# Kernel tuning notes

Hardware: AMD Instinct MI355X
Metric: run time of the kernel (lower is better)

## Reference

```python
import jax, jax.numpy as jnp
import numpy as np

B, T, S = 64, 32, 64          # batch, tgt_len, src_len
V, E, H, C = 32000, 512, 1024, 2048  # vocab, emb, hidden, context (2*d_model)


def setup_inputs() -> dict:
    key = jax.random.key(0)
    ks = jax.random.split(key, 16)
    g = lambda i, shape, s=0.05: jax.random.normal(ks[i], shape, jnp.float32) * s
    return dict(
        y=jax.random.randint(ks[0], (B, T), 0, V),
        context=g(1, (B, S, C), 1.0),
        context_mask=jnp.zeros((B, S), jnp.int32),  # 1 = padding
        hidden=g(2, (B, H), 1.0),
        emb=g(3, (V, E)),
        W_ih1=g(4, (3 * H, E)), W_hh1=g(5, (3 * H, H)),
        b_ih1=jnp.zeros((3 * H,), jnp.float32), b_hh1=jnp.zeros((3 * H,), jnp.float32),
        Wq=g(6, (H, H)), bq=jnp.zeros((H,), jnp.float32),
        Wk=g(7, (C, H)), v_attn=g(8, (H,)),
        W_ih2=g(9, (3 * H, C)), W_hh2=g(10, (3 * H, H)),
        b_ih2=jnp.zeros((3 * H,), jnp.float32), b_hh2=jnp.zeros((3 * H,), jnp.float32),
        Wi=g(11, (E, E)), bi=jnp.zeros((E,), jnp.float32),
        Wh=g(12, (E, H)), bh=jnp.zeros((E,), jnp.float32),
        Wc=g(13, (E, C)), bc=jnp.zeros((E,), jnp.float32),
    )


def gru_cell(x, h, W_ih, W_hh, b_ih, b_hh):
    gi = x @ W_ih.T + b_ih
    gh = h @ W_hh.T + b_hh
    i_r, i_z, i_n = jnp.split(gi, 3, axis=-1)
    h_r, h_z, h_n = jnp.split(gh, 3, axis=-1)
    r = jax.nn.sigmoid(i_r + h_r)
    z = jax.nn.sigmoid(i_z + h_z)
    n = jnp.tanh(i_n + r * h_n)
    return (1.0 - z) * n + z * h


def reference(y, context, context_mask, hidden, emb,
              W_ih1, W_hh1, b_ih1, b_hh1,
              Wq, bq, Wk, v_attn,
              W_ih2, W_hh2, b_ih2, b_hh2,
              Wi, bi, Wh, bh, Wc, bc):
    x = emb[y]                                        # [B,T,E]
    cache = jnp.einsum('bsc,ch->bsh', context, Wk)    # attention key cache
    pad = context_mask.astype(bool)
    neg = jnp.finfo(x.dtype).min

    def step(h, x_t):
        h1 = gru_cell(x_t, h, W_ih1, W_hh1, b_ih1, b_hh1)        # [B,H]
        q = h1 @ Wq + bq                                          # [B,H]
        scores = jnp.einsum('bsh,h->bs', jnp.tanh(q[:, None, :] + cache), v_attn)
        probs = jax.nn.softmax(jnp.where(pad, neg, scores), axis=-1)
        attn = jnp.einsum('bs,bsc->bc', probs, context)           # [B,C]
        h2 = gru_cell(attn, h1, W_ih2, W_hh2, b_ih2, b_hh2)
        return h2, (h2, attn)

    h_final, (out, attn) = jax.lax.scan(step, hidden, jnp.swapaxes(x, 0, 1))
    out = jnp.swapaxes(out, 0, 1)                     # [B,T,H]
    attn = jnp.swapaxes(attn, 0, 1)                   # [B,T,C]
    logits = jnp.tanh(x @ Wi.T + bi + out @ Wh.T + bh + attn @ Wc.T + bc)
    return logits, h_final
```

## Files before the change

kernel.cpp:

```cpp
#include <hip/hip_runtime.h>
#include <math.h>

#define B_ 64
#define T_ 32
#define S_ 64
#define E_ 512
#define H_ 1024
#define C_ 2048
#define G_ 3072
#define NBLK 256
#define FLSTR 16

typedef __bf16 bf16_t;
typedef bf16_t bf16x8 __attribute__((ext_vector_type(8)));
typedef float f32x4 __attribute__((ext_vector_type(4)));
typedef unsigned long long u64;

__device__ __forceinline__ float sigm_(float x) { return 1.f / (1.f + __expf(-x)); }
__device__ __forceinline__ float tanh_(float x) { return 1.f - 2.f / (__expf(2.f * x) + 1.f); }

__device__ __forceinline__ unsigned short bits_(bf16_t x)
{
    union { bf16_t b; unsigned short u; } c; c.b = x; return c.u;
}
__device__ __forceinline__ void astore_pair(bf16_t* p, bf16_t lo, bf16_t hi)
{
    unsigned u = (unsigned)bits_(lo) | ((unsigned)bits_(hi) << 16);
    __hip_atomic_store((unsigned*)p, u, __ATOMIC_RELAXED, __HIP_MEMORY_SCOPE_AGENT);
}
__device__ __forceinline__ void astore_f32(float* p, float v)
{
    union { float f; unsigned u; } c; c.f = v;
    __hip_atomic_store((unsigned*)p, c.u, __ATOMIC_RELAXED, __HIP_MEMORY_SCOPE_AGENT);
}

__device__ __forceinline__ void split8(const float* __restrict__ p, bf16x8& h, bf16x8& l)
{
    float4 a = *(const float4*)p;
    float4 b = *(const float4*)(p + 4);
    float v[8] = {a.x, a.y, a.z, a.w, b.x, b.y, b.z, b.w};
    #pragma unroll
    for (int q = 0; q < 8; ++q) {
        h[q] = (bf16_t)v[q];
        l[q] = (bf16_t)(v[q] - (float)h[q]);
    }
}

__global__ __launch_bounds__(256)
void embed_kernel(const int* __restrict__ y, const float* __restrict__ emb,
                  float* __restrict__ x)
{
    int i = blockIdx.x * 256 + threadIdx.x;
    int row = i / (E_ / 4);
    int e4  = i % (E_ / 4);
    const float4* src = (const float4*)(emb + (size_t)y[row] * E_);
    ((float4*)(x + (size_t)row * E_))[e4] = src[e4];
}

__global__ void transpose_kernel(const float* __restrict__ in, float* __restrict__ out,
                                 int R, int Ccols)
{
    __shared__ float t[32][33];
    int r0 = blockIdx.y * 32, c0 = blockIdx.x * 32;
    t[threadIdx.y][threadIdx.x] = in[(size_t)(r0 + threadIdx.y) * Ccols + c0 + threadIdx.x];
    __syncthreads();
    out[(size_t)(c0 + threadIdx.y) * R + r0 + threadIdx.x] = t[threadIdx.x][threadIdx.y];
}

__global__ __launch_bounds__(256)
void cvt_ctx(const float* __restrict__ in, bf16_t* __restrict__ out)
{
    int i = blockIdx.x * 256 + threadIdx.x;
    const float4* s4 = (const float4*)in + 2 * i;
    float4 a = s4[0], b = s4[1];
    bf16x8 o;
    o[0] = (bf16_t)a.x; o[1] = (bf16_t)a.y; o[2] = (bf16_t)a.z; o[3] = (bf16_t)a.w;
    o[4] = (bf16_t)b.x; o[5] = (bf16_t)b.y; o[6] = (bf16_t)b.z; o[7] = (bf16_t)b.w;
    ((bf16x8*)out)[i] = o;
}

#define LSTR 80

template<int ACCUM, int PERM>
__global__ __launch_bounds__(256)
void sgemm(const float* __restrict__ A, const float* __restrict__ Wt,
           float* __restrict__ out, int N, int K)
{
    __shared__ char AH[128 * LSTR];
    __shared__ char AL[128 * LSTR];
    __shared__ char WH[128 * LSTR];
    __shared__ char WL[128 * LSTR];
    const int tid = threadIdx.x;
    const int lane = tid & 63, wave = tid >> 6;
    const int m0 = blockIdx.y * 128, n0 = blockIdx.x * 128;
    const int wm = (wave & 1) * 64, wn = (wave >> 1) * 64;
    const int l15 = lane & 15, l4 = lane >> 4;

    f32x4 acc[4][4] = {};

    for (int k0 = 0; k0 < K; k0 += 32) {
        #pragma unroll
        for (int p = 0; p < 2; ++p) {
            int e = tid + p * 256;
            int row = e >> 2, ch = e & 3;
            int off = row * LSTR + ch * 16;
            bf16x8 h, l;
            split8(A + (size_t)(m0 + row) * K + k0 + ch * 8, h, l);
            *(bf16x8*)(AH + off) = h; *(bf16x8*)(AL + off) = l;
            split8(Wt + (size_t)(n0 + row) * K + k0 + ch * 8, h, l);
            *(bf16x8*)(WH + off) = h; *(bf16x8*)(WL + off) = l;
        }
        __syncthreads();
        bf16x8 ah[4], al[4], wh[4], wl[4];
        #pragma unroll
        for (int i = 0; i < 4; ++i) {
            int off = (wm + i * 16 + l15) * LSTR + l4 * 16;
            ah[i] = *(const bf16x8*)(AH + off);
            al[i] = *(const bf16x8*)(AL + off);
        }
        #pragma unroll
        for (int j = 0; j < 4; ++j) {
            int off = (wn + j * 16 + l15) * LSTR + l4 * 16;
            wh[j] = *(const bf16x8*)(WH + off);
            wl[j] = *(const bf16x8*)(WL + off);
        }
        #pragma unroll
        for (int i = 0; i < 4; ++i)
            #pragma unroll
            for (int j = 0; j < 4; ++j) {
                acc[i][j] = __builtin_amdgcn_mfma_f32_16x16x32_bf16(ah[i], wh[j], acc[i][j], 0, 0, 0);
                acc[i][j] = __builtin_amdgcn_mfma_f32_16x16x32_bf16(ah[i], wl[j], acc[i][j], 0, 0, 0);
                acc[i][j] = __builtin_amdgcn_mfma_f32_16x16x32_bf16(al[i], wh[j], acc[i][j], 0, 0, 0);
            }
        __syncthreads();
    }

    #pragma unroll
    for (int i = 0; i < 4; ++i)
        #pragma unroll
        for (int j = 0; j < 4; ++j)
            #pragma unroll
            for (int r = 0; r < 4; ++r) {
                int m = m0 + wm + i * 16 + l4 * 4 + r;
                int n = n0 + wn + j * 16 + l15;
                if (PERM) {
                    int b = m >> 5, t = m & 31;
                    int gate = n >> 10, jj = n & 1023;
                    size_t dst = (((size_t)(jj >> 2) * 32 + t) * 64 + b) * 12
                                 + gate * 4 + (jj & 3);
                    out[dst] = acc[i][j][r];
                } else if (ACCUM) {
                    out[(size_t)m * N + n] += acc[i][j][r];
                } else {
                    out[(size_t)m * N + n] = acc[i][j][r];
                }
            }
}

#define W1H_OFF 0
#define W1L_OFF 24576
#define W3H_OFF 49152
#define W2H_OFF 98304
#define W2L_OFF 131072
#define SMEM_BYTES 163840

__device__ __forceinline__ void gbar(unsigned* flags, unsigned* done,
                                     unsigned epoch, int blk, int tid)
{
    asm volatile("s_waitcnt vmcnt(0)" ::: "memory");
    __syncthreads();
    if (blk == 0) {
        if (tid > 0 && tid < NBLK) {
            while (__hip_atomic_load(&flags[tid * FLSTR], __ATOMIC_RELAXED,
                                     __HIP_MEMORY_SCOPE_AGENT) < epoch)
                __builtin_amdgcn_s_sleep(4);
        }
        __syncthreads();
        if (tid < 8)
            __hip_atomic_store(&done[tid * FLSTR], epoch, __ATOMIC_RELAXED,
                               __HIP_MEMORY_SCOPE_AGENT);
        __syncthreads();
    } else {
        if (tid == 0) {
            __hip_atomic_store(&flags[blk * FLSTR], epoch, __ATOMIC_RELAXED,
                               __HIP_MEMORY_SCOPE_AGENT);
            while (__hip_atomic_load(&done[(blk & 7) * FLSTR], __ATOMIC_RELAXED,
                                     __HIP_MEMORY_SCOPE_AGENT) < epoch)
                __builtin_amdgcn_s_sleep(4);
        }
        __syncthreads();
    }
}

__global__ __launch_bounds__(1024, 4)
void scan_kernel(
    const float* __restrict__ Whh1, const float* __restrict__ Whh2,
    const float* __restrict__ WqT,  const float* __restrict__ Wih2,
    const float* __restrict__ xg2,
    const float* __restrict__ b_ih1, const float* __restrict__ b_hh1,
    const float* __restrict__ b_ih2, const float* __restrict__ b_hh2,
    const float* __restrict__ bq,    const float* __restrict__ v_attn,
    const int*   __restrict__ cmask,
    const float* __restrict__ hidden,
    const float* __restrict__ cacheK, const bf16_t* __restrict__ ctxb,
    float* __restrict__ qgv, float* __restrict__ hf,
    bf16_t* __restrict__ h1H, bf16_t* __restrict__ h1L,
    float* __restrict__ attnseq, float* __restrict__ outseq,
    float* __restrict__ hfinal,
    float* __restrict__ scgv,
    unsigned* __restrict__ flags, unsigned* __restrict__ done)
{
    extern __shared__ char sm[];
    const int tid = threadIdx.x, blk = blockIdx.x;
    const int lane = tid & 63, wave = tid >> 6;
    const int l15 = lane & 15, l4 = lane >> 4;
    const int blk4 = blk * 4;
    const int ab  = blk & 63;
    const int aq  = blk >> 6;

    if (tid == 0) __builtin_amdgcn_fence(__ATOMIC_ACQUIRE, "agent");
    __syncthreads();

    for (int e = tid; e < 12 * 128; e += 1024) {
        int r = e >> 7, c = e & 127;
        bf16x8 h, l;
        split8(Whh1 + (size_t)((r >> 2) * 1024 + blk4 + (r & 3)) * 1024 + c * 8, h, l);
        int off = r * 2048 + ((c * 16) ^ ((r & 7) << 4));
        *(bf16x8*)(sm + W1H_OFF + off) = h;
        *(bf16x8*)(sm + W1L_OFF + off) = l;
    }
    for (int e = tid; e < 16 * 128; e += 1024) {
        int r = e >> 7, c = e & 127;
        const float* src = (r < 12)
            ? Whh2 + (size_t)((r >> 2) * 1024 + blk4 + (r & 3)) * 1024 + c * 8
            : WqT + (size_t)(blk4 + r - 12) * 1024 + c * 8;
        bf16x8 h, l;
        split8(src, h, l);
        int off = r * 2048 + ((c * 16) ^ ((r & 7) << 4));
        *(bf16x8*)(sm + W2H_OFF + off) = h;
        *(bf16x8*)(sm + W2L_OFF + off) = l;
    }
    for (int e = tid; e < 12 * 256; e += 1024) {
        int r = e >> 8, c = e & 255;
        bf16x8 h, l;
        split8(Wih2 + (size_t)((r >> 2) * 1024 + blk4 + (r & 3)) * 2048 + c * 8, h, l);
        *(bf16x8*)(sm + W3H_OFF + r * 4096 + ((c * 16) ^ ((r & 7) << 4))) = h;
    }

    const int j = blk4 + l15;
    if (wave < 4 && l15 < 4) {
        #pragma unroll
        for (int r2 = 0; r2 < 4; ++r2) {
            int b = wave * 16 + l4 * 4 + r2;
            hf[b * 1024 + j] = hidden[b * 1024 + j];
        }
    }

    float vreg[16], bqreg[16];
    #pragma unroll
    for (int i = 0; i < 16; ++i) {
        vreg[i]  = v_attn[lane + 64 * i];
        bqreg[i] = bq[lane + 64 * i];
    }
    float ckreg[16];
    {
        const float* ck = cacheK + ((size_t)ab * 64 + aq * 16 + wave) * 1024;
        #pragma unroll
        for (int i = 0; i < 16; ++i) ckreg[i] = ck[lane + 64 * i];
    }
    const int cmy = aq * 512 + (tid >> 1);
    const int sbase = (tid & 1) * 32;
    unsigned cr[16];
    {
        const bf16_t* cb = ctxb + ((size_t)ab * 64 + sbase) * 2048 + cmy;
        #pragma unroll
        for (int q = 0; q < 16; ++q) {
            unsigned lo = bits_(cb[(size_t)(2 * q) * 2048]);
            unsigned hi = bits_(cb[(size_t)(2 * q + 1) * 2048]);
            cr[q] = lo | (hi << 16);
        }
    }

    float bi1r = 0, bi1z = 0, bi1n = 0, bh1r = 0, bh1z = 0, bh1n = 0;
    float bi2r = 0, bi2z = 0, bi2n = 0, bh2r = 0, bh2z = 0, bh2n = 0;
    if (wave < 4 && l15 < 4) {
        bi1r = b_ih1[j]; bi1z = b_ih1[1024 + j]; bi1n = b_ih1[2048 + j];
        bh1r = b_hh1[j]; bh1z = b_hh1[1024 + j]; bh1n = b_hh1[2048 + j];
        bi2r = b_ih2[j]; bi2z = b_ih2[1024 + j]; bi2n = b_ih2[2048 + j];
        bh2r = b_hh2[j]; bh2z = b_hh2[1024 + j]; bh2n = b_hh2[2048 + j];
    }

    unsigned epoch = 0;
    gbar(flags, done, ++epoch, blk, tid);

    float h1r_[4] = {0.f, 0.f, 0.f, 0.f};
    f32x4 acc1 = {0.f, 0.f, 0.f, 0.f};

    for (int t = 0; t < T_; ++t) {
        if (wave < 4) {
            f32x4 acc0 = {0.f, 0.f, 0.f, 0.f};
            const int brow = wave * 16 + l15;
            const float* asrc = (t == 0) ? hidden + (size_t)brow * 1024
                                         : outseq + ((size_t)brow * T_ + t - 1) * 1024;
            #pragma unroll 8
            for (int kk = 0; kk < 32; ++kk) {
                bf16x8 avh, avl;
                split8(asrc + kk * 32 + l4 * 8, avh, avl);
                int boff = (kk * 64 + l4 * 16) ^ ((l15 & 7) << 4);
                bf16x8 bvh = *(const bf16x8*)(sm + W1H_OFF + l15 * 2048 + boff);
                bf16x8 bvl = *(const bf16x8*)(sm + W1L_OFF + l15 * 2048 + boff);
                acc0 = __builtin_amdgcn_mfma_f32_16x16x32_bf16(avh, bvh, acc0, 0, 0, 0);
                acc0 = __builtin_amdgcn_mfma_f32_16x16x32_bf16(avl, bvh, acc0, 0, 0, 0);
                acc0 = __builtin_amdgcn_mfma_f32_16x16x32_bf16(avh, bvl, acc0, 0, 0, 0);
            }
            const float* xg = xg2 + (((size_t)blk * 32 + t) * 64) * 12;
            #pragma unroll
            for (int r2 = 0; r2 < 4; ++r2) {
                float gr = acc0[r2];
                float gz = __shfl(acc0[r2], (lane & 48) | (l15 + 4), 64);
                float gn = __shfl(acc0[r2], (lane & 48) | (l15 + 8), 64);
                float h1v = 0.f;
                int b = wave * 16 + l4 * 4 + r2;
                if (l15 < 4) {
                    float rr = sigm_(xg[b * 12 + l15]     + bi1r + gr + bh1r);
                    float zz = sigm_(xg[b * 12 + 4 + l15] + bi1z + gz + bh1z);
                    float nn = tanh_(xg[b * 12 + 8 + l15] + bi1n + rr * (gn + bh1n));
                    h1v = (1.f - zz) * nn + zz * hf[b * 1024 + j];
                    h1r_[r2] = h1v;
                }
                float h1o = __shfl(h1v, lane + 1, 64);
                if (l15 < 4 && (l15 & 1) == 0) {
                    bf16_t hS = (bf16_t)h1v, hO = (bf16_t)h1o;
                    size_t vo = ((size_t)t * 64 + b) * 1024 + j;
                    astore_pair(h1H + vo, hS, hO);
                    astore_pair(h1L + vo,
                                (bf16_t)(h1v - (float)hS), (bf16_t)(h1o - (float)hO));
                }
            }
        }
        gbar(flags, done, ++epoch, blk, tid);

        if (wave < 4) {
            acc1 = (f32x4){0.f, 0.f, 0.f, 0.f};
            const int brow = wave * 16 + l15;
            const bf16_t* ah = h1H + ((size_t)t * 64 + brow) * 1024;
            const bf16_t* al = h1L + ((size_t)t * 64 + brow) * 1024;
            #pragma unroll 8
            for (int kk = 0; kk < 32; ++kk) {
                bf16x8 avh = *(const bf16x8*)(ah + kk * 32 + l4 * 8);
                bf16x8 avl = *(const bf16x8*)(al + kk * 32 + l4 * 8);
                int boff = (kk * 64 + l4 * 16) ^ ((l15 & 7) << 4);
                bf16x8 bvh = *(const bf16x8*)(sm + W2H_OFF + l15 * 2048 + boff);
                bf16x8 bvl = *(const bf16x8*)(sm + W2L_OFF + l15 * 2048 + boff);
                acc1 = __builtin_amdgcn_mfma_f32_16x16x32_bf16(avh, bvh, acc1, 0, 0, 0);
                acc1 = __builtin_amdgcn_mfma_f32_16x16x32_bf16(avl, bvh, acc1, 0, 0, 0);
                acc1 = __builtin_amdgcn_mfma_f32_16x16x32_bf16(avh, bvl, acc1, 0, 0, 0);
            }
            if (l15 >= 12) {
                int jq = blk4 + l15 - 12;
                #pragma unroll
                for (int r2 = 0; r2 < 4; ++r2)
                    astore_f32(&qgv[((size_t)t * 64 + (wave * 16 + l4 * 4 + r2)) * 1024 + jq],
                               acc1[r2]);
            }
        }
        gbar(flags, done, ++epoch, blk, tid);

        {
            const float* qrow = qgv + ((size_t)t * 64 + ab) * 1024;
            float sum = 0.f;
            #pragma unroll
            for (int i = 0; i < 16; ++i)
                sum += tanh_(qrow[lane + 64 * i] + bqreg[i] + ckreg[i]) * vreg[i];
            #pragma unroll
            for (int off = 32; off; off >>= 1) sum += __shfl_down(sum, off, 64);
            if (lane == 0) astore_f32(&scgv[(size_t)t * 4096 + ab * 64 + aq * 16 + wave], sum);
        }
        gbar(flags, done, ++epoch, blk, tid);

        {
            const float* scrow = scgv + (size_t)t * 4096 + ab * 64;
            float v = (cmask[ab * 64 + lane] != 0) ? -3.4e38f : scrow[lane];
            float mx = v;
            #pragma unroll
            for (int off = 32; off; off >>= 1) mx = fmaxf(mx, __shfl_xor(mx, off, 64));
            float e = __expf(v - mx);
            float sden = e;
            #pragma unroll
            for (int off = 32; off; off >>= 1) sden += __shfl_xor(sden, off, 64);
            float prv = e / sden;

            float sum = 0.f;
            #pragma unroll
            for (int q = 0; q < 16; ++q) {
                float p0 = __shfl(prv, sbase + 2 * q, 64);
                float p1 = __shfl(prv, sbase + 2 * q + 1, 64);
                sum += p0 * __uint_as_float(cr[q] << 16);
                sum += p1 * __uint_as_float(cr[q] & 0xffff0000u);
            }
            sum += __shfl_xor(sum, 1, 64);
            if ((tid & 1) == 0)
                astore_f32(attnseq + ((size_t)ab * T_ + t) * 2048 + cmy, sum);
        }
        gbar(flags, done, ++epoch, blk, tid);

        if (wave < 4) {
            f32x4 acc3 = {0.f, 0.f, 0.f, 0.f};
            const int brow = wave * 16 + l15;
            const float* aptr = attnseq + ((size_t)brow * T_ + t) * 2048;
            #pragma unroll 8
            for (int kk = 0; kk < 64; ++kk) {
                bf16x8 avh, avl;
                split8(aptr + kk * 32 + l4 * 8, avh, avl);
                bf16x8 bvh = *(const bf16x8*)(sm + W3H_OFF + l15 * 4096 +
                                              ((kk * 64 + l4 * 16) ^ ((l15 & 7) << 4)));
                acc3 = __builtin_amdgcn_mfma_f32_16x16x32_bf16(avh, bvh, acc3, 0, 0, 0);
                acc3 = __builtin_amdgcn_mfma_f32_16x16x32_bf16(avl, bvh, acc3, 0, 0, 0);
            }
            #pragma unroll
            for (int r2 = 0; r2 < 4; ++r2) {
                float ir  = acc3[r2];
                float iz  = __shfl(acc3[r2], (lane & 48) | (l15 + 4), 64);
                float in2 = __shfl(acc3[r2], (lane & 48) | (l15 + 8), 64);
                float hr  = acc1[r2];
                float hz  = __shfl(acc1[r2], (lane & 48) | (l15 + 4), 64);
                float hn  = __shfl(acc1[r2], (lane & 48) | (l15 + 8), 64);
                int b = wave * 16 + l4 * 4 + r2;
                if (l15 < 4) {
                    float rr = sigm_(ir + bi2r + hr + bh2r);
                    float zz = sigm_(iz + bi2z + hz + bh2z);
                    float nn = tanh_(in2 + bi2n + rr * (hn + bh2n));
                    float h2 = (1.f - zz) * nn + zz * h1r_[r2];
                    hf[b * 1024 + j] = h2;
                    astore_f32(&outseq[((size_t)b * T_ + t) * 1024 + j], h2);
                    if (t == T_ - 1) hfinal[b * 1024 + j] = h2;
                }
            }
        }
        gbar(flags, done, ++epoch, blk, tid);
    }
}

__global__ __launch_bounds__(256)
void final_kernel(const float* __restrict__ Lacc,
                  const float* __restrict__ bi, const float* __restrict__ bh,
                  const float* __restrict__ bc, float* __restrict__ out)
{
    int i = blockIdx.x * 256 + threadIdx.x;
    int e = i & 511;
    out[i] = tanh_(Lacc[i] + bi[e] + bh[e] + bc[e]);
}

extern "C" void kernel_launch(void* const* d_in, const int* in_sizes, int n_in,
                              void* d_out, int out_size, void* d_ws, size_t ws_size,
                              hipStream_t stream)
{
    const int*   y       = (const int*)  d_in[0];
    const float* context = (const float*)d_in[1];
    const int*   cmask   = (const int*)  d_in[2];
    const float* hidden  = (const float*)d_in[3];
    const float* emb     = (const float*)d_in[4];
    const float* W_ih1   = (const float*)d_in[5];
    const float* W_hh1   = (const float*)d_in[6];
    const float* b_ih1   = (const float*)d_in[7];
    const float* b_hh1   = (const float*)d_in[8];
    const float* Wq      = (const float*)d_in[9];
    const float* bq      = (const float*)d_in[10];
    const float* Wk      = (const float*)d_in[11];
    const float* v_attn  = (const float*)d_in[12];
    const float* W_ih2   = (const float*)d_in[13];
    const float* W_hh2   = (const float*)d_in[14];
    const float* b_ih2   = (const float*)d_in[15];
    const float* b_hh2   = (const float*)d_in[16];
    const float* Wi      = (const float*)d_in[17];
    const float* bi      = (const float*)d_in[18];
    const float* Wh      = (const float*)d_in[19];
    const float* bh      = (const float*)d_in[20];
    const float* Wc      = (const float*)d_in[21];
    const float* bc      = (const float*)d_in[22];

    char* ws = (char*)d_ws;
    size_t o = 0;
    auto alloc = [&](size_t bytes) { char* p = ws + o; o += (bytes + 255) & ~(size_t)255; return p; };
    unsigned* flags = (unsigned*)alloc(NBLK * FLSTR * 4);
    unsigned* done  = (unsigned*)alloc(8 * FLSTR * 4);
    float*  x       = (float*) alloc((size_t)2048 * 512 * 4);
    float*  WkT     = (float*) alloc((size_t)1024 * 2048 * 4);
    float*  WqT     = (float*) alloc((size_t)1024 * 1024 * 4);
    bf16_t* ctxb    = (bf16_t*)alloc((size_t)4096 * 2048 * 2);
    float*  xg2     = (float*) alloc((size_t)2048 * 3072 * 4);
    float*  Lacc    = (float*) alloc((size_t)2048 * 512 * 4);
    float*  cacheK  = (float*) alloc((size_t)4096 * 1024 * 4);
    float*  qgv     = (float*) alloc((size_t)T_ * 64 * 1024 * 4);
    float*  hf      = (float*) alloc((size_t)64 * 1024 * 4);
    bf16_t* h1H     = (bf16_t*)alloc((size_t)T_ * 64 * 1024 * 2);
    bf16_t* h1L     = (bf16_t*)alloc((size_t)T_ * 64 * 1024 * 2);
    float*  attnseq = (float*) alloc((size_t)2048 * 2048 * 4);
    float*  outseq  = (float*) alloc((size_t)2048 * 1024 * 4);
    float*  scgv    = (float*) alloc((size_t)T_ * 64 * 64 * 4);

    hipMemsetAsync(flags, 0, (NBLK * FLSTR + 8 * FLSTR) * 4, stream);

    embed_kernel<<<(B_*T_*E_/4 + 255)/256, 256, 0, stream>>>(y, emb, x);
    transpose_kernel<<<dim3(1024/32, 2048/32), dim3(32,32), 0, stream>>>(Wk, WkT, 2048, 1024);
    transpose_kernel<<<dim3(1024/32, 1024/32), dim3(32,32), 0, stream>>>(Wq, WqT, 1024, 1024);
    cvt_ctx<<<(4096*2048/8)/256, 256, 0, stream>>>(context, ctxb);

    sgemm<0, 1><<<dim3(G_/128, 16), 256, 0, stream>>>(x, W_ih1, xg2, G_, E_);
    sgemm<0, 0><<<dim3(E_/128, 16), 256, 0, stream>>>(x, Wi, Lacc, E_, E_);
    sgemm<0, 0><<<dim3(H_/128, 32), 256, 0, stream>>>(context, WkT, cacheK, H_, C_);

    hipFuncSetAttribute((const void*)scan_kernel, hipFuncAttributeMaxDynamicSharedMemorySize, SMEM_BYTES);
    scan_kernel<<<NBLK, 1024, SMEM_BYTES, stream>>>(
        W_hh1, W_hh2, WqT, W_ih2, xg2,
        b_ih1, b_hh1, b_ih2, b_hh2, bq, v_attn, cmask, hidden, cacheK, ctxb,
        qgv, hf, h1H, h1L, attnseq, outseq,
        (float*)d_out + (size_t)B_ * T_ * E_, scgv, flags, done);

    sgemm<1, 0><<<dim3(E_/128, 16), 256, 0, stream>>>(outseq, Wh, Lacc, E_, H_);
    sgemm<1, 0><<<dim3(E_/128, 16), 256, 0, stream>>>(attnseq, Wc, Lacc, E_, C_);

    final_kernel<<<(B_*T_*E_)/256, 256, 0, stream>>>(Lacc, bi, bh, bc, (float*)d_out);
}
```

Measured before the change: 3.134 ms.

## Split-K across all 16 waves in scan GEMMs and fuse score phase

Each per-step MFMA GEMM (GRU1 hidden, GRU2 hidden/query, GRU2 input) now splits its K range across four wave groups. Partials are reduced through a per-block global scratch buffer behind a block-level sync, so all 16 waves do matmul work instead of only 4. The attention score computation now has each block compute all 64 source scores for its batch row locally, which removes one grid-wide barrier per timestep and the global score buffer. The query bias is folded into the stored q. This trades extra __syncthreads, scratch traffic and redundant cacheK reads for shorter serial critical paths.

```diff
diff --git a/kernel.cpp b/kernel.cpp
--- a/kernel.cpp
+++ b/kernel.cpp
@@ -207,7 +207,7 @@
     bf16_t* __restrict__ h1H, bf16_t* __restrict__ h1L,
     float* __restrict__ attnseq, float* __restrict__ outseq,
     float* __restrict__ hfinal,
-    float* __restrict__ scgv,
+    float* __restrict__ red,
     unsigned* __restrict__ flags, unsigned* __restrict__ done)
 {
     extern __shared__ char sm[];
@@ -217,6 +217,9 @@
     const int blk4 = blk * 4;
     const int ab  = blk & 63;
     const int aq  = blk >> 6;
+    const int kg  = wave >> 2;
+    const int bg  = wave & 3;
+    float* redp = red + (size_t)blk * 4096;
 
     if (tid == 0) __builtin_amdgcn_fence(__ATOMIC_ACQUIRE, "agent");
     __syncthreads();
@@ -256,18 +259,9 @@
         }
     }
 
-    float vreg[16], bqreg[16];
+    float vreg[16];
     #pragma unroll
-    for (int i = 0; i < 16; ++i) {
-        vreg[i]  = v_attn[lane + 64 * i];
-        bqreg[i] = bq[lane + 64 * i];
-    }
-    float ckreg[16];
-    {
-        const float* ck = cacheK + ((size_t)ab * 64 + aq * 16 + wave) * 1024;
-        #pragma unroll
-        for (int i = 0; i < 16; ++i) ckreg[i] = ck[lane + 64 * i];
-    }
+    for (int i = 0; i < 16; ++i) vreg[i] = v_attn[lane + 64 * i];
     const int cmy = aq * 512 + (tid >> 1);
     const int sbase = (tid & 1) * 32;
     unsigned cr[16];
@@ -283,12 +277,14 @@
 
     float bi1r = 0, bi1z = 0, bi1n = 0, bh1r = 0, bh1z = 0, bh1n = 0;
     float bi2r = 0, bi2z = 0, bi2n = 0, bh2r = 0, bh2z = 0, bh2n = 0;
+    float bqv = 0.f;
     if (wave < 4 && l15 < 4) {
         bi1r = b_ih1[j]; bi1z = b_ih1[1024 + j]; bi1n = b_ih1[2048 + j];
         bh1r = b_hh1[j]; bh1z = b_hh1[1024 + j]; bh1n = b_hh1[2048 + j];
         bi2r = b_ih2[j]; bi2z = b_ih2[1024 + j]; bi2n = b_ih2[2048 + j];
         bh2r = b_hh2[j]; bh2z = b_hh2[1024 + j]; bh2n = b_hh2[2048 + j];
     }
+    if (wave < 4 && l15 >= 12) bqv = bq[blk4 + l15 - 12];
 
     unsigned epoch = 0;
     gbar(flags, done, ++epoch, blk, tid);
@@ -297,90 +293,115 @@
     f32x4 acc1 = {0.f, 0.f, 0.f, 0.f};
 
     for (int t = 0; t < T_; ++t) {
-        if (wave < 4) {
-            f32x4 acc0 = {0.f, 0.f, 0.f, 0.f};
-            const int brow = wave * 16 + l15;
+        {
+            f32x4 a0 = {0.f, 0.f, 0.f, 0.f};
+            const int brow = bg * 16 + l15;
             const float* asrc = (t == 0) ? hidden + (size_t)brow * 1024
                                          : outseq + ((size_t)brow * T_ + t - 1) * 1024;
-            #pragma unroll 8
-            for (int kk = 0; kk < 32; ++kk) {
+            #pragma unroll
+            for (int kq = 0; kq < 8; ++kq) {
+                int kk = kg * 8 + kq;
                 bf16x8 avh, avl;
                 split8(asrc + kk * 32 + l4 * 8, avh, avl);
                 int boff = (kk * 64 + l4 * 16) ^ ((l15 & 7) << 4);
                 bf16x8 bvh = *(const bf16x8*)(sm + W1H_OFF + l15 * 2048 + boff);
                 bf16x8 bvl = *(const bf16x8*)(sm + W1L_OFF + l15 * 2048 + boff);
-                acc0 = __builtin_amdgcn_mfma_f32_16x16x32_bf16(avh, bvh, acc0, 0, 0, 0);
-                acc0 = __builtin_amdgcn_mfma_f32_16x16x32_bf16(avl, bvh, acc0, 0, 0, 0);
-                acc0 = __builtin_amdgcn_mfma_f32_16x16x32_bf16(avh, bvl, acc0, 0, 0, 0);
-            }
-            const float* xg = xg2 + (((size_t)blk * 32 + t) * 64) * 12;
-            #pragma unroll
-            for (int r2 = 0; r2 < 4; ++r2) {
-                float gr = acc0[r2];
-                float gz = __shfl(acc0[r2], (lane & 48) | (l15 + 4), 64);
-                float gn = __shfl(acc0[r2], (lane & 48) | (l15 + 8), 64);
-                float h1v = 0.f;
-                int b = wave * 16 + l4 * 4 + r2;
-                if (l15 < 4) {
-                    float rr = sigm_(xg[b * 12 + l15]     + bi1r + gr + bh1r);
-                    float zz = sigm_(xg[b * 12 + 4 + l15] + bi1z + gz + bh1z);
-                    float nn = tanh_(xg[b * 12 + 8 + l15] + bi1n + rr * (gn + bh1n));
-                    h1v = (1.f - zz) * nn + zz * hf[b * 1024 + j];
-                    h1r_[r2] = h1v;
-                }
-                float h1o = __shfl(h1v, lane + 1, 64);
-                if (l15 < 4 && (l15 & 1) == 0) {
-                    bf16_t hS = (bf16_t)h1v, hO = (bf16_t)h1o;
-                    size_t vo = ((size_t)t * 64 + b) * 1024 + j;
-                    astore_pair(h1H + vo, hS, hO);
-                    astore_pair(h1L + vo,
-                                (bf16_t)(h1v - (float)hS), (bf16_t)(h1o - (float)hO));
+                a0 = __builtin_amdgcn_mfma_f32_16x16x32_bf16(avh, bvh, a0, 0, 0, 0);
+                a0 = __builtin_amdgcn_mfma_f32_16x16x32_bf16(avl, bvh, a0, 0, 0, 0);
+                a0 = __builtin_amdgcn_mfma_f32_16x16x32_bf16(avh, bvl, a0, 0, 0, 0);
+            }
+            if (kg) *(f32x4*)(redp + (size_t)wave * 256 + lane * 4) = a0;
+            __syncthreads();
+            if (wave < 4) {
+                #pragma unroll
+                for (int g = 1; g < 4; ++g) {
+                    f32x4 p = *(const f32x4*)(redp + (size_t)(g * 4 + wave) * 256 + lane * 4);
+                    a0[0] += p[0]; a0[1] += p[1]; a0[2] += p[2]; a0[3] += p[3];
+                }
+                const float* xg = xg2 + (((size_t)blk * 32 + t) * 64) * 12;
+                #pragma unroll
+                for (int r2 = 0; r2 < 4; ++r2) {
+                    float gr = a0[r2];
+                    float gz = __shfl(a0[r2], (lane & 48) | (l15 + 4), 64);
+                    float gn = __shfl(a0[r2], (lane & 48) | (l15 + 8), 64);
+                    float h1v = 0.f;
+                    int b = wave * 16 + l4 * 4 + r2;
+                    if (l15 < 4) {
+                        float rr = sigm_(xg[b * 12 + l15]     + bi1r + gr + bh1r);
+                        float zz = sigm_(xg[b * 12 + 4 + l15] + bi1z + gz + bh1z);
+                        float nn = tanh_(xg[b * 12 + 8 + l15] + bi1n + rr * (gn + bh1n));
+                        h1v = (1.f - zz) * nn + zz * hf[b * 1024 + j];
+                        h1r_[r2] = h1v;
+                    }
+                    float h1o = __shfl(h1v, lane + 1, 64);
+                    if (l15 < 4 && (l15 & 1) == 0) {
+                        bf16_t hS = (bf16_t)h1v, hO = (bf16_t)h1o;
+                        size_t vo = ((size_t)t * 64 + b) * 1024 + j;
+                        astore_pair(h1H + vo, hS, hO);
+                        astore_pair(h1L + vo,
+                                    (bf16_t)(h1v - (float)hS), (bf16_t)(h1o - (float)hO));
+                    }
                 }
             }
         }
         gbar(flags, done, ++epoch, blk, tid);
 
-        if (wave < 4) {
-            acc1 = (f32x4){0.f, 0.f, 0.f, 0.f};
-            const int brow = wave * 16 + l15;
+        {
+            f32x4 a1 = {0.f, 0.f, 0.f, 0.f};
+            const int brow = bg * 16 + l15;
             const bf16_t* ah = h1H + ((size_t)t * 64 + brow) * 1024;
             const bf16_t* al = h1L + ((size_t)t * 64 + brow) * 1024;
-            #pragma unroll 8
-            for (int kk = 0; kk < 32; ++kk) {
+            #pragma unroll
+            for (int kq = 0; kq < 8; ++kq) {
+                int kk = kg * 8 + kq;
                 bf16x8 avh = *(const bf16x8*)(ah + kk * 32 + l4 * 8);
                 bf16x8 avl = *(const bf16x8*)(al + kk * 32 + l4 * 8);
                 int boff = (kk * 64 + l4 * 16) ^ ((l15 & 7) << 4);
                 bf16x8 bvh = *(const bf16x8*)(sm + W2H_OFF + l15 * 2048 + boff);
                 bf16x8 bvl = *(const bf16x8*)(sm + W2L_OFF + l15 * 2048 + boff);
-                acc1 = __builtin_amdgcn_mfma_f32_16x16x32_bf16(avh, bvh, acc1, 0, 0, 0);
-                acc1 = __builtin_amdgcn_mfma_f32_16x16x32_bf16(avl, bvh, acc1, 0, 0, 0);
-                acc1 = __builtin_amdgcn_mfma_f32_16x16x32_bf16(avh, bvl, acc1, 0, 0, 0);
-            }
-            if (l15 >= 12) {
-                int jq = blk4 + l15 - 12;
-                #pragma unroll
-                for (int r2 = 0; r2 < 4; ++r2)
-                    astore_f32(&qgv[((size_t)t * 64 + (wave * 16 + l4 * 4 + r2)) * 1024 + jq],
-                               acc1[r2]);
+                a1 = __builtin_amdgcn_mfma_f32_16x16x32_bf16(avh, bvh, a1, 0, 0, 0);
+                a1 = __builtin_amdgcn_mfma_f32_16x16x32_bf16(avl, bvh, a1, 0, 0, 0);
+                a1 = __builtin_amdgcn_mfma_f32_16x16x32_bf16(avh, bvl, a1, 0, 0, 0);
+            }
+            if (kg) *(f32x4*)(redp + (size_t)wave * 256 + lane * 4) = a1;
+            __syncthreads();
+            if (wave < 4) {
+                acc1 = a1;
+                #pragma unroll
+                for (int g = 1; g < 4; ++g) {
+                    f32x4 p = *(const f32x4*)(redp + (size_t)(g * 4 + wave) * 256 + lane * 4);
+                    acc1[0] += p[0]; acc1[1] += p[1]; acc1[2] += p[2]; acc1[3] += p[3];
+                }
+                if (l15 >= 12) {
+                    int jq = blk4 + l15 - 12;
+                    #pragma unroll
+                    for (int r2 = 0; r2 < 4; ++r2)
+                        astore_f32(&qgv[((size_t)t * 64 + (wave * 16 + l4 * 4 + r2)) * 1024 + jq],
+                                   acc1[r2] + bqv);
+                }
             }
         }
         gbar(flags, done, ++epoch, blk, tid);
 
         {
             const float* qrow = qgv + ((size_t)t * 64 + ab) * 1024;
-            float sum = 0.f;
-            #pragma unroll
-            for (int i = 0; i < 16; ++i)
-                sum += tanh_(qrow[lane + 64 * i] + bqreg[i] + ckreg[i]) * vreg[i];
-            #pragma unroll
-            for (int off = 32; off; off >>= 1) sum += __shfl_down(sum, off, 64);
-            if (lane == 0) astore_f32(&scgv[(size_t)t * 4096 + ab * 64 + aq * 16 + wave], sum);
-        }
-        gbar(flags, done, ++epoch, blk, tid);
-
-        {
-            const float* scrow = scgv + (size_t)t * 4096 + ab * 64;
-            float v = (cmask[ab * 64 + lane] != 0) ? -3.4e38f : scrow[lane];
+            float qreg[16];
+            #pragma unroll
+            for (int i = 0; i < 16; ++i) qreg[i] = qrow[lane + 64 * i];
+            #pragma unroll
+            for (int sl = 0; sl < 4; ++sl) {
+                int s = wave * 4 + sl;
+                const float* ck = cacheK + ((size_t)ab * 64 + s) * 1024;
+                float sum = 0.f;
+                #pragma unroll
+                for (int i = 0; i < 16; ++i)
+                    sum += tanh_(qreg[i] + ck[lane + 64 * i]) * vreg[i];
+                #pragma unroll
+                for (int off = 32; off; off >>= 1) sum += __shfl_down(sum, off, 64);
+                if (lane == 0) redp[s] = sum;
+            }
+            __syncthreads();
+            float v = (cmask[ab * 64 + lane] != 0) ? -3.4e38f : redp[lane];
             float mx = v;
             #pragma unroll
             for (int off = 32; off; off >>= 1) mx = fmaxf(mx, __shfl_xor(mx, off, 64));
@@ -404,36 +425,46 @@
         }
         gbar(flags, done, ++epoch, blk, tid);
 
-        if (wave < 4) {
-            f32x4 acc3 = {0.f, 0.f, 0.f, 0.f};
-            const int brow = wave * 16 + l15;
+        {
+            f32x4 a3 = {0.f, 0.f, 0.f, 0.f};
+            const int brow = bg * 16 + l15;
             const float* aptr = attnseq + ((size_t)brow * T_ + t) * 2048;
-            #pragma unroll 8
-            for (int kk = 0; kk < 64; ++kk) {
+            #pragma unroll
+            for (int kq = 0; kq < 16; ++kq) {
+                int kk = kg * 16 + kq;
                 bf16x8 avh, avl;
                 split8(aptr + kk * 32 + l4 * 8, avh, avl);
                 bf16x8 bvh = *(const bf16x8*)(sm + W3H_OFF + l15 * 4096 +
                                               ((kk * 64 + l4 * 16) ^ ((l15 & 7) << 4)));
-                acc3 = __builtin_amdgcn_mfma_f32_16x16x32_bf16(avh, bvh, acc3, 0, 0, 0);
-                acc3 = __builtin_amdgcn_mfma_f32_16x16x32_bf16(avl, bvh, acc3, 0, 0, 0);
-            }
-            #pragma unroll
-            for (int r2 = 0; r2 < 4; ++r2) {
-                float ir  = acc3[r2];
-                float iz  = __shfl(acc3[r2], (lane & 48) | (l15 + 4), 64);
-                float in2 = __shfl(acc3[r2], (lane & 48) | (l15 + 8), 64);
-                float hr  = acc1[r2];
-                float hz  = __shfl(acc1[r2], (lane & 48) | (l15 + 4), 64);
-                float hn  = __shfl(acc1[r2], (lane & 48) | (l15 + 8), 64);
-                int b = wave * 16 + l4 * 4 + r2;
-                if (l15 < 4) {
-                    float rr = sigm_(ir + bi2r + hr + bh2r);
-                    float zz = sigm_(iz + bi2z + hz + bh2z);
-                    float nn = tanh_(in2 + bi2n + rr * (hn + bh2n));
-                    float h2 = (1.f - zz) * nn + zz * h1r_[r2];
-                    hf[b * 1024 + j] = h2;
-                    astore_f32(&outseq[((size_t)b * T_ + t) * 1024 + j], h2);
-                    if (t == T_ - 1) hfinal[b * 1024 + j] = h2;
+                a3 = __builtin_amdgcn_mfma_f32_16x16x32_bf16(avh, bvh, a3, 0, 0, 0);
+                a3 = __builtin_amdgcn_mfma_f32_16x16x32_bf16(avl, bvh, a3, 0, 0, 0);
+            }
+            if (kg) *(f32x4*)(redp + (size_t)wave * 256 + lane * 4) = a3;
+            __syncthreads();
+            if (wave < 4) {
+                #pragma unroll
+                for (int g = 1; g < 4; ++g) {
+                    f32x4 p = *(const f32x4*)(redp + (size_t)(g * 4 + wave) * 256 + lane * 4);
+                    a3[0] += p[0]; a3[1] += p[1]; a3[2] += p[2]; a3[3] += p[3];
+                }
+                #pragma unroll
+                for (int r2 = 0; r2 < 4; ++r2) {
+                    float ir  = a3[r2];
+                    float iz  = __shfl(a3[r2], (lane & 48) | (l15 + 4), 64);
+                    float in2 = __shfl(a3[r2], (lane & 48) | (l15 + 8), 64);
+                    float hr  = acc1[r2];
+                    float hz  = __shfl(acc1[r2], (lane & 48) | (l15 + 4), 64);
+                    float hn  = __shfl(acc1[r2], (lane & 48) | (l15 + 8), 64);
+                    int b = wave * 16 + l4 * 4 + r2;
+                    if (l15 < 4) {
+                        float rr = sigm_(ir + bi2r + hr + bh2r);
+                        float zz = sigm_(iz + bi2z + hz + bh2z);
+                        float nn = tanh_(in2 + bi2n + rr * (hn + bh2n));
+                        float h2 = (1.f - zz) * nn + zz * h1r_[r2];
+                        hf[b * 1024 + j] = h2;
+                        astore_f32(&outseq[((size_t)b * T_ + t) * 1024 + j], h2);
+                        if (t == T_ - 1) hfinal[b * 1024 + j] = h2;
+                    }
                 }
             }
         }
@@ -497,7 +528,7 @@
     bf16_t* h1L     = (bf16_t*)alloc((size_t)T_ * 64 * 1024 * 2);
     float*  attnseq = (float*) alloc((size_t)2048 * 2048 * 4);
     float*  outseq  = (float*) alloc((size_t)2048 * 1024 * 4);
-    float*  scgv    = (float*) alloc((size_t)T_ * 64 * 64 * 4);
+    float*  red     = (float*) alloc((size_t)NBLK * 4096 * 4);
 
     hipMemsetAsync(flags, 0, (NBLK * FLSTR + 8 * FLSTR) * 4, stream);
 
@@ -515,7 +546,7 @@
         W_hh1, W_hh2, WqT, W_ih2, xg2,
         b_ih1, b_hh1, b_ih2, b_hh2, bq, v_attn, cmask, hidden, cacheK, ctxb,
         qgv, hf, h1H, h1L, attnseq, outseq,
-        (float*)d_out + (size_t)B_ * T_ * E_, scgv, flags, done);
+        (float*)d_out + (size_t)B_ * T_ * E_, red, flags, done);
 
     sgemm<1, 0><<<dim3(E_/128, 16), 256, 0, stream>>>(outseq, Wh, Lacc, E_, H_);
     sgemm<1, 0><<<dim3(E_/128, 16), 256, 0, stream>>>(attnseq, Wc, Lacc, E_, C_);
```

Result: slower. 3.577 ms (+14.1%).

## Compute all attention scores per batch in-block to remove a grid barrier

Applied to the files above, without the earlier changes.

Each block now computes all 64 source scores for its batch row instead of only 16, so the softmax no longer has to wait for other blocks. That removes one grid-wide barrier per timestep and the global score exchange buffer. The trade is four times the tanh work per block, 64 cache registers per thread instead of 16, and redundant score computation across the four blocks that share a batch. The bq bias is folded into the q store, and scores go through a per-block global scratch buffer synchronised with __syncthreads.

```diff
diff --git a/kernel.cpp b/kernel.cpp
--- a/kernel.cpp
+++ b/kernel.cpp
@@ -207,7 +207,7 @@
     bf16_t* __restrict__ h1H, bf16_t* __restrict__ h1L,
     float* __restrict__ attnseq, float* __restrict__ outseq,
     float* __restrict__ hfinal,
-    float* __restrict__ scgv,
+    float* __restrict__ red,
     unsigned* __restrict__ flags, unsigned* __restrict__ done)
 {
     extern __shared__ char sm[];
@@ -217,6 +217,7 @@
     const int blk4 = blk * 4;
     const int ab  = blk & 63;
     const int aq  = blk >> 6;
+    float* redp = red + (size_t)blk * 1024;
 
     if (tid == 0) __builtin_amdgcn_fence(__ATOMIC_ACQUIRE, "agent");
     __syncthreads();
@@ -256,17 +257,15 @@
         }
     }
 
-    float vreg[16], bqreg[16];
+    float vreg[16];
     #pragma unroll
-    for (int i = 0; i < 16; ++i) {
-        vreg[i]  = v_attn[lane + 64 * i];
-        bqreg[i] = bq[lane + 64 * i];
-    }
-    float ckreg[16];
-    {
-        const float* ck = cacheK + ((size_t)ab * 64 + aq * 16 + wave) * 1024;
-        #pragma unroll
-        for (int i = 0; i < 16; ++i) ckreg[i] = ck[lane + 64 * i];
+    for (int i = 0; i < 16; ++i) vreg[i] = v_attn[lane + 64 * i];
+    float ckreg[4][16];
+    #pragma unroll
+    for (int sl = 0; sl < 4; ++sl) {
+        const float* ck = cacheK + ((size_t)ab * 64 + wave * 4 + sl) * 1024;
+        #pragma unroll
+        for (int i = 0; i < 16; ++i) ckreg[sl][i] = ck[lane + 64 * i];
     }
     const int cmy = aq * 512 + (tid >> 1);
     const int sbase = (tid & 1) * 32;
@@ -283,12 +282,14 @@
 
     float bi1r = 0, bi1z = 0, bi1n = 0, bh1r = 0, bh1z = 0, bh1n = 0;
     float bi2r = 0, bi2z = 0, bi2n = 0, bh2r = 0, bh2z = 0, bh2n = 0;
+    float bqv = 0.f;
     if (wave < 4 && l15 < 4) {
         bi1r = b_ih1[j]; bi1z = b_ih1[1024 + j]; bi1n = b_ih1[2048 + j];
         bh1r = b_hh1[j]; bh1z = b_hh1[1024 + j]; bh1n = b_hh1[2048 + j];
         bi2r = b_ih2[j]; bi2z = b_ih2[1024 + j]; bi2n = b_ih2[2048 + j];
         bh2r = b_hh2[j]; bh2z = b_hh2[1024 + j]; bh2n = b_hh2[2048 + j];
     }
+    if (wave < 4 && l15 >= 12) bqv = bq[blk4 + l15 - 12];
 
     unsigned epoch = 0;
     gbar(flags, done, ++epoch, blk, tid);
@@ -361,26 +362,29 @@
                 #pragma unroll
                 for (int r2 = 0; r2 < 4; ++r2)
                     astore_f32(&qgv[((size_t)t * 64 + (wave * 16 + l4 * 4 + r2)) * 1024 + jq],
-                               acc1[r2]);
+                               acc1[r2] + bqv);
             }
         }
         gbar(flags, done, ++epoch, blk, tid);
 
         {
             const float* qrow = qgv + ((size_t)t * 64 + ab) * 1024;
-            float sum = 0.f;
-            #pragma unroll
-            for (int i = 0; i < 16; ++i)
-                sum += tanh_(qrow[lane + 64 * i] + bqreg[i] + ckreg[i]) * vreg[i];
-            #pragma unroll
-            for (int off = 32; off; off >>= 1) sum += __shfl_down(sum, off, 64);
-            if (lane == 0) astore_f32(&scgv[(size_t)t * 4096 + ab * 64 + aq * 16 + wave], sum);
-        }
-        gbar(flags, done, ++epoch, blk, tid);
-
-        {
-            const float* scrow = scgv + (size_t)t * 4096 + ab * 64;
-            float v = (cmask[ab * 64 + lane] != 0) ? -3.4e38f : scrow[lane];
+            float qreg[16];
+            #pragma unroll
+            for (int i = 0; i < 16; ++i) qreg[i] = qrow[lane + 64 * i];
+            #pragma unroll
+            for (int sl = 0; sl < 4; ++sl) {
+                float sum = 0.f;
+                #pragma unroll
+                for (int i = 0; i < 16; ++i)
+                    sum += tanh_(qreg[i] + ckreg[sl][i]) * vreg[i];
+                #pragma unroll
+                for (int off = 32; off; off >>= 1) sum += __shfl_down(sum, off, 64);
+                if (lane == 0) redp[wave * 4 + sl] = sum;
+            }
+            asm volatile("s_waitcnt vmcnt(0)" ::: "memory");
+            __syncthreads();
+            float v = (cmask[ab * 64 + lane] != 0) ? -3.4e38f : redp[lane];
             float mx = v;
             #pragma unroll
             for (int off = 32; off; off >>= 1) mx = fmaxf(mx, __shfl_xor(mx, off, 64));
@@ -497,7 +501,7 @@
     bf16_t* h1L     = (bf16_t*)alloc((size_t)T_ * 64 * 1024 * 2);
     float*  attnseq = (float*) alloc((size_t)2048 * 2048 * 4);
     float*  outseq  = (float*) alloc((size_t)2048 * 1024 * 4);
-    float*  scgv    = (float*) alloc((size_t)T_ * 64 * 64 * 4);
+    float*  red     = (float*) alloc((size_t)NBLK * 1024 * 4);
 
     hipMemsetAsync(flags, 0, (NBLK * FLSTR + 8 * FLSTR) * 4, stream);
 
@@ -515,7 +519,7 @@
         W_hh1, W_hh2, WqT, W_ih2, xg2,
         b_ih1, b_hh1, b_ih2, b_hh2, bq, v_attn, cmask, hidden, cacheK, ctxb,
         qgv, hf, h1H, h1L, attnseq, outseq,
-        (float*)d_out + (size_t)B_ * T_ * E_, scgv, flags, done);
+        (float*)d_out + (size_t)B_ * T_ * E_, red, flags, done);
 
     sgemm<1, 0><<<dim3(E_/128, 16), 256, 0, stream>>>(outseq, Wh, Lacc, E_, H_);
     sgemm<1, 0><<<dim3(E_/128, 16), 256, 0, stream>>>(attnseq, Wc, Lacc, E_, C_);
```

Measured after the change: 3.546 ms. 1.13x slower.

## Prefetch next-phase operands into cache using idle waves and fold bq into q

Applied to the files above, without the earlier changes.

The idle waves (4-15) now read the data the next phase will consume, such as previous outputs, h1 split buffers and attention vectors, and discard the sums. The goal is to warm the cache so the active waves see fewer misses after each grid barrier. The query bias is added once when q is written, instead of being held in per-thread registers for every score. The key cache rows are loaded from memory inside the step rather than kept in registers, which frees registers at the cost of extra loads. The prefetches add memory traffic that may compete with the active waves.

```diff
diff --git a/kernel.cpp b/kernel.cpp
--- a/kernel.cpp
+++ b/kernel.cpp
@@ -256,18 +256,9 @@
         }
     }
 
-    float vreg[16], bqreg[16];
+    float vreg[16];
     #pragma unroll
-    for (int i = 0; i < 16; ++i) {
-        vreg[i]  = v_attn[lane + 64 * i];
-        bqreg[i] = bq[lane + 64 * i];
-    }
-    float ckreg[16];
-    {
-        const float* ck = cacheK + ((size_t)ab * 64 + aq * 16 + wave) * 1024;
-        #pragma unroll
-        for (int i = 0; i < 16; ++i) ckreg[i] = ck[lane + 64 * i];
-    }
+    for (int i = 0; i < 16; ++i) vreg[i] = v_attn[lane + 64 * i];
     const int cmy = aq * 512 + (tid >> 1);
     const int sbase = (tid & 1) * 32;
     unsigned cr[16];
@@ -283,12 +274,14 @@
 
     float bi1r = 0, bi1z = 0, bi1n = 0, bh1r = 0, bh1z = 0, bh1n = 0;
     float bi2r = 0, bi2z = 0, bi2n = 0, bh2r = 0, bh2z = 0, bh2n = 0;
+    float bqv = 0.f;
     if (wave < 4 && l15 < 4) {
         bi1r = b_ih1[j]; bi1z = b_ih1[1024 + j]; bi1n = b_ih1[2048 + j];
         bh1r = b_hh1[j]; bh1z = b_hh1[1024 + j]; bh1n = b_hh1[2048 + j];
         bi2r = b_ih2[j]; bi2z = b_ih2[1024 + j]; bi2n = b_ih2[2048 + j];
         bh2r = b_hh2[j]; bh2z = b_hh2[1024 + j]; bh2n = b_hh2[2048 + j];
     }
+    if (wave < 4 && l15 >= 12) bqv = bq[blk4 + l15 - 12];
 
     unsigned epoch = 0;
     gbar(flags, done, ++epoch, blk, tid);
@@ -337,6 +330,27 @@
                                 (bf16_t)(h1v - (float)hS), (bf16_t)(h1o - (float)hO));
                 }
             }
+        } else {
+            int pid = tid - 256;
+            float accp = 0.f;
+            if (t == 0) {
+                const float4* src = (const float4*)hidden;
+                for (int i = pid; i < 16384; i += 768) {
+                    float4 v = src[i];
+                    accp += v.x + v.y + v.z + v.w;
+                }
+            } else {
+                for (int i = pid; i < 16384; i += 768) {
+                    int row = i >> 8, c4 = i & 255;
+                    float4 v = ((const float4*)(outseq + ((size_t)row * T_ + t - 1) * 1024))[c4];
+                    accp += v.x + v.y + v.z + v.w;
+                }
+            }
+            if (pid < 192) {
+                float4 v = ((const float4*)(xg2 + (((size_t)blk * 32 + t) * 64) * 12))[pid];
+                accp += v.x + v.y + v.z + v.w;
+            }
+            asm volatile("" :: "v"(accp));
         }
         gbar(flags, done, ++epoch, blk, tid);
 
@@ -361,20 +375,32 @@
                 #pragma unroll
                 for (int r2 = 0; r2 < 4; ++r2)
                     astore_f32(&qgv[((size_t)t * 64 + (wave * 16 + l4 * 4 + r2)) * 1024 + jq],
-                               acc1[r2]);
-            }
+                               acc1[r2] + bqv);
+            }
+        } else {
+            int pid = tid - 256;
+            float accp = 0.f;
+            const float4* s1 = (const float4*)(h1H + (size_t)t * 65536);
+            const float4* s2 = (const float4*)(h1L + (size_t)t * 65536);
+            for (int i = pid; i < 8192; i += 768) {
+                float4 a = s1[i], b = s2[i];
+                accp += a.x + a.w + b.x + b.w;
+            }
+            asm volatile("" :: "v"(accp));
         }
         gbar(flags, done, ++epoch, blk, tid);
 
         {
+            int s = aq * 16 + wave;
             const float* qrow = qgv + ((size_t)t * 64 + ab) * 1024;
+            const float* ck = cacheK + ((size_t)ab * 64 + s) * 1024;
             float sum = 0.f;
             #pragma unroll
             for (int i = 0; i < 16; ++i)
-                sum += tanh_(qrow[lane + 64 * i] + bqreg[i] + ckreg[i]) * vreg[i];
+                sum += tanh_(qrow[lane + 64 * i] + ck[lane + 64 * i]) * vreg[i];
             #pragma unroll
             for (int off = 32; off; off >>= 1) sum += __shfl_down(sum, off, 64);
-            if (lane == 0) astore_f32(&scgv[(size_t)t * 4096 + ab * 64 + aq * 16 + wave], sum);
+            if (lane == 0) astore_f32(&scgv[(size_t)t * 4096 + ab * 64 + s], sum);
         }
         gbar(flags, done, ++epoch, blk, tid);
 
@@ -436,6 +462,15 @@
                     if (t == T_ - 1) hfinal[b * 1024 + j] = h2;
                 }
             }
+        } else {
+            int pid = tid - 256;
+            float accp = 0.f;
+            for (int i = pid; i < 32768; i += 768) {
+                int row = i >> 9, c4 = i & 511;
+                float4 v = ((const float4*)(attnseq + ((size_t)row * T_ + t) * 2048))[c4];
+                accp += v.x + v.y + v.z + v.w;
+            }
+            asm volatile("" :: "v"(accp));
         }
         gbar(flags, done, ++epoch, blk, tid);
     }
```

After: 2.875 ms, median of 2. -8.3%, faster.
